# Kernel optimization log

Hardware: AMD Instinct MI355X
Metric: run time of the kernel (lower is better)

## Reference

```python
import jax, jax.numpy as jnp
import numpy as np

B, S, E, H = 2, 2048, 1024, 16
HD = E // H
SCALE = 1.0 / np.sqrt(HD)
PR_QKV = 0.05   # precision_ratio for q/k/v (critical_attention=False)
PR_OUT = 0.10
ROUTE_THR = 0.05  # gradient_threshold (critical_attention=False)
LN_EPS = 1e-5


def rpb_linear(x, W, b, precision_ratio):
    """ResidualPrecisionBoostLinear: ternary-quantized weight (threshold 0.7*mean|W|,
    per-tensor scale) plus top-`precision_ratio` fraction of residual kept full precision."""
    absW = jnp.abs(W)
    thr = 0.7 * jnp.mean(absW)
    tmask = (absW > thr).astype(W.dtype)
    scale = jnp.sum(absW * tmask) / jnp.maximum(jnp.sum(tmask), 1.0)
    Wq = scale * jnp.sign(W) * tmask
    res = W - Wq
    k = int(precision_ratio * W.size)
    kth = jax.lax.top_k(jnp.abs(res).ravel(), k)[0][-1]
    W_eff = Wq + res * (jnp.abs(res) >= kth).astype(W.dtype)
    return x @ W_eff.T + b


def selective_route(x, threshold):
    # forward: zero out small-magnitude activations (straight-through in training)
    return x * (jnp.abs(x) >= threshold).astype(x.dtype)


def layer_norm(x, g, b):
    mu = jnp.mean(x, axis=-1, keepdims=True)
    var = jnp.mean(jnp.square(x - mu), axis=-1, keepdims=True)
    return (x - mu) * jax.lax.rsqrt(var + LN_EPS) * g + b


def setup_inputs() -> dict:
    key = jax.random.key(0)
    ks = jax.random.split(key, 12)
    f = lambda k, shp, s=1.0: jax.random.normal(k, shp, dtype=jnp.float32) * s
    return {
        "query": f(ks[0], (B, S, E)),
        "key": f(ks[1], (B, S, E)),
        "value": f(ks[2], (B, S, E)),
        "Wq": f(ks[3], (E, E), 0.02), "bq": jnp.zeros((E,), jnp.float32),
        "Wk": f(ks[4], (E, E), 0.02), "bk": jnp.zeros((E,), jnp.float32),
        "Wv": f(ks[5], (E, E), 0.02), "bv": jnp.zeros((E,), jnp.float32),
        "Wo": f(ks[6], (E, E), 0.02), "bo": jnp.zeros((E,), jnp.float32),
        "ln_g": jnp.ones((E,), jnp.float32),
        "ln_b": jnp.zeros((E,), jnp.float32),
    }


def reference(query, key, value, Wq, bq, Wk, bk, Wv, bv, Wo, bo, ln_g, ln_b):
    qn = layer_norm(query, ln_g, ln_b)
    q = selective_route(rpb_linear(qn, Wq, bq, PR_QKV), ROUTE_THR)
    k = selective_route(rpb_linear(key, Wk, bk, PR_QKV), ROUTE_THR)
    v = selective_route(rpb_linear(value, Wv, bv, PR_QKV), ROUTE_THR)
    # [B,S,E] -> [B,H,S,HD]
    q = q.reshape(B, S, H, HD).transpose(0, 2, 1, 3)
    k = k.reshape(B, S, H, HD).transpose(0, 2, 1, 3)
    v = v.reshape(B, S, H, HD).transpose(0, 2, 1, 3)
    scores = jnp.einsum("bhqd,bhkd->bhqk", q, k) * SCALE
    attn = jax.nn.softmax(scores, axis=-1)   # dropout is identity in eval
    ctx = jnp.einsum("bhqk,bhkd->bhqd", attn, v)
    ctx = ctx.transpose(0, 2, 1, 3).reshape(B, S, E)
    return rpb_linear(ctx, Wo, bo, PR_OUT)
```

## Files before the change

kernel.cpp:

```cpp
#include <hip/hip_runtime.h>
#include <stdio.h>
#include <stdint.h>

#define BB 2
#define SS 2048
#define ED 1024
#define HH 16
#define HDD 64
#define MROWS 4096
#define NW_ELEM 1048576u

typedef unsigned short ushortT;
typedef __attribute__((ext_vector_type(8))) short bf16x8;
typedef __attribute__((ext_vector_type(4))) float f32x4;
typedef __attribute__((ext_vector_type(16))) float f32x16;

#define U_WHI 0u
#define U_WLO 4194304u
#define U_XQ  8388608u
#define U_XK  12582912u
#define U_XV  16777216u
#define U_QH  20971520u
#define U_KH  25165824u
#define U_VH  29360128u
#define LP_OFF  33554432u
#define P0_OFF  67108864u
#define P1_OFF  83886080u
#define SMALL_OFF  100663296u
#define HIST_OFF   SMALL_OFF
#define ABS_OFF    (SMALL_OFF + 16384u)
#define MSK_OFF    (ABS_OFF + 32u)
#define CNT_OFF    (MSK_OFF + 32u)
#define SMALL_BYTES 16464u
#define WS_NEEDED  (SMALL_OFF + SMALL_BYTES)

#define SC44 17592186044416.0f
#define INV44 (1.0 / 17592186044416.0)
#define QSCALE 0.18033688011112042f

__device__ __forceinline__ const float* wsel(int w, const float* W0, const float* W1,
                                             const float* W2, const float* W3) {
  return w == 0 ? W0 : w == 1 ? W1 : w == 2 ? W2 : W3;
}

__device__ __forceinline__ ushortT f2bf(float x) {
  unsigned u = __float_as_uint(x);
  unsigned r = (u + 0x7FFFu + ((u >> 16) & 1u)) >> 16;
  return (ushortT)r;
}
__device__ __forceinline__ float bf2f(ushortT b) {
  return __uint_as_float(((unsigned)b) << 16);
}
__device__ __forceinline__ void bsplit(float x, ushortT& h, ushortT& l) {
  ushortT hb = f2bf(x);
  float hf = bf2f(hb);
  h = hb;
  l = f2bf(x - hf);
}
__device__ __forceinline__ unsigned pkbf(float a, float b) {
  unsigned r;
  asm("v_cvt_pk_bf16_f32 %0, %1, %2" : "=v"(r) : "v"(a), "v"(b));
  return r;
}
__device__ __forceinline__ void plswap(unsigned& a, unsigned& b) {
  asm("v_permlane32_swap_b32 %0, %1" : "+v"(a), "+v"(b));
}
__device__ __forceinline__ float fexp2(float x) {
#if __has_builtin(__builtin_amdgcn_exp2f)
  return __builtin_amdgcn_exp2f(x);
#else
  float r;
  asm("v_exp_f32 %0, %1\n\ts_nop 1" : "=v"(r) : "v"(x));
  return r;
#endif
}

__device__ __forceinline__ void gld_lds16(const ushortT* g, ushortT* s) {
  __builtin_amdgcn_global_load_lds((__attribute__((address_space(1))) void*)g,
                                   (__attribute__((address_space(3))) void*)s, 16, 0, 0);
}

template <int N> __device__ __forceinline__ void waitv() {
  if constexpr (N == 0) asm volatile("s_waitcnt vmcnt(0)" ::: "memory");
  else if constexpr (N == 4) asm volatile("s_waitcnt vmcnt(4)" ::: "memory");
  else if constexpr (N == 6) asm volatile("s_waitcnt vmcnt(6)" ::: "memory");
}
__device__ __forceinline__ void pipe_barrier() {
  __builtin_amdgcn_s_barrier();
  __builtin_amdgcn_sched_barrier(0);
}

__device__ __forceinline__ float get_thr(const unsigned long long* sAbs, int w) {
  return 0.7f * (float)((double)sAbs[w] * INV44 / 1048576.0);
}
__device__ __forceinline__ float get_scale(const unsigned long long* sMsk,
                                           const unsigned* cnt, int w) {
  double s = (double)sMsk[w] * INV44;
  return (float)s / fmaxf((float)cnt[w], 1.0f);
}

__device__ __forceinline__ void scan_sel(const unsigned* hist, unsigned& k, unsigned& prefix,
                                         unsigned* sh, int t) {
  sh[t] = hist[t];
  __syncthreads();
  for (int off = 1; off < 256; off <<= 1) {
    unsigned add = (t + off < 256) ? sh[t + off] : 0u;
    __syncthreads();
    sh[t] += add;
    __syncthreads();
  }
  int sel = __syncthreads_count((int)(sh[t] >= k)) - 1;
  unsigned suf = sh[sel];
  k -= (suf - hist[sel]);
  prefix = (prefix << 8) | (unsigned)sel;
  __syncthreads();
}

__device__ __forceinline__ void ln_unit(const float* __restrict__ query,
                                        const float* __restrict__ g,
                                        const float* __restrict__ b,
                                        ushortT* __restrict__ Xq,
                                        int row, int t, float* red) {
  float4 v = *(const float4*)&query[(size_t)row * ED + t * 4];
  float s = v.x + v.y + v.z + v.w;
#pragma unroll
  for (int m = 32; m; m >>= 1) s += __shfl_xor(s, m, 64);
  if ((t & 63) == 0) red[t >> 6] = s;
  __syncthreads();
  float mu = (red[0] + red[1] + red[2] + red[3]) * (1.0f / 1024.0f);
  float dx = v.x - mu, dy = v.y - mu, dz = v.z - mu, dw = v.w - mu;
  float s2 = dx * dx + dy * dy + dz * dz + dw * dw;
#pragma unroll
  for (int m = 32; m; m >>= 1) s2 += __shfl_xor(s2, m, 64);
  if ((t & 63) == 0) red[4 + (t >> 6)] = s2;
  __syncthreads();
  float var = (red[4] + red[5] + red[6] + red[7]) * (1.0f / 1024.0f);
  float inv = rsqrtf(var + 1e-5f);
  float4 gg = *(const float4*)&g[t * 4];
  float4 bb = *(const float4*)&b[t * 4];
  float ys[4] = {dx * inv * gg.x + bb.x, dy * inv * gg.y + bb.y,
                 dz * inv * gg.z + bb.z, dw * inv * gg.w + bb.w};
  ushort4 h4;
#pragma unroll
  for (int c = 0; c < 4; c++) ((ushortT*)&h4)[c] = f2bf(ys[c]);
  *(ushort4*)&Xq[(size_t)row * ED + t * 4] = h4;
}

__device__ __forceinline__ void cast_unit(const float* __restrict__ src,
                                          ushortT* __restrict__ dst, int idx, int t) {
  const int i = (idx * 256 + t) * 4;
  float4 v = *(const float4*)&src[i];
  ushort4 h4;
  h4.x = f2bf(v.x); h4.y = f2bf(v.y); h4.z = f2bf(v.z); h4.w = f2bf(v.w);
  *(ushort4*)&dst[i] = h4;
}

__global__ __launch_bounds__(256) void k_pre(const float* __restrict__ query,
                                             const float* __restrict__ key,
                                             const float* __restrict__ value,
                                             const float* __restrict__ g,
                                             const float* __restrict__ b,
                                             const float* W0, const float* W1,
                                             const float* W2, const float* W3,
                                             ushortT* __restrict__ Xq,
                                             ushortT* __restrict__ Xk,
                                             ushortT* __restrict__ Xv,
                                             unsigned long long* sAbs) {
  const int t = threadIdx.x, bid = blockIdx.x;
  __shared__ float red[8];
  __shared__ unsigned long long sd[256];
  if (bid < 4096) {
    ln_unit(query, g, b, Xq, bid, t, red);
  } else if (bid < 8192) {
    cast_unit(key, Xk, bid - 4096, t);
  } else if (bid < 12288) {
    cast_unit(value, Xv, bid - 8192, t);
  } else {
    const int c = bid - 12288, w = c >> 8;
    const float* W = wsel(w, W0, W1, W2, W3) + (c & 255) * 4096;
    unsigned long long s = 0;
#pragma unroll
    for (int r = 0; r < 4; r++) {
      float4 v = *(const float4*)(W + (t + 256 * r) * 4);
      s += (unsigned long long)(fabsf(v.x) * SC44);
      s += (unsigned long long)(fabsf(v.y) * SC44);
      s += (unsigned long long)(fabsf(v.z) * SC44);
      s += (unsigned long long)(fabsf(v.w) * SC44);
    }
    sd[t] = s;
    __syncthreads();
    for (int off = 128; off > 0; off >>= 1) {
      if (t < off) sd[t] += sd[t + off];
      __syncthreads();
    }
    if (!t) atomicAdd(&sAbs[w], sd[0]);
  }
}

__global__ __launch_bounds__(256) void k_masked(const float* W0, const float* W1,
                                                const float* W2, const float* W3,
                                                const unsigned long long* sAbs,
                                                unsigned long long* sMsk, unsigned* sCnt) {
  const int w = blockIdx.y, t = threadIdx.x;
  const float thr = get_thr(sAbs, w);
  const float* W = wsel(w, W0, W1, W2, W3) + blockIdx.x * 4096;
  unsigned long long s = 0;
  unsigned c = 0;
#pragma unroll
  for (int r = 0; r < 4; r++) {
    float4 v = *(const float4*)(W + (t + 256 * r) * 4);
    float xs[4] = {v.x, v.y, v.z, v.w};
#pragma unroll
    for (int q = 0; q < 4; q++) {
      float a = fabsf(xs[q]);
      if (a > thr) { s += (unsigned long long)(a * SC44); c++; }
    }
  }
  __shared__ unsigned long long sd[256];
  __shared__ unsigned sc[256];
  sd[t] = s; sc[t] = c;
  __syncthreads();
  for (int off = 128; off > 0; off >>= 1) {
    if (t < off) { sd[t] += sd[t + off]; sc[t] += sc[t + off]; }
    __syncthreads();
  }
  if (!t) { atomicAdd(&sMsk[w], sd[0]); atomicAdd(&sCnt[w], sc[0]); }
}

__global__ __launch_bounds__(256) void k_hist(const float* W0, const float* W1,
                                              const float* W2, const float* W3,
                                              const unsigned long long* sAbs,
                                              const unsigned long long* sMsk,
                                              const unsigned* sCnt,
                                              unsigned* histG, int pass) {
  const int w = blockIdx.y, t = threadIdx.x;
  __shared__ unsigned sh[256];
  __shared__ unsigned h[256];
  const float thr = get_thr(sAbs, w);
  const float scale = get_scale(sMsk, sCnt, w);
  unsigned k = (w == 3) ? 104857u : 52428u, prefix = 0u;
  for (int pp = 0; pp < pass; pp++)
    scan_sel(histG + (pp * 4 + w) * 256, k, prefix, sh, t);

  h[t] = 0;
  __syncthreads();
  const float* W = wsel(w, W0, W1, W2, W3) + blockIdx.x * 4096;
  const int shift1 = 32 - 8 * pass;
  const int shift2 = 24 - 8 * pass;
#pragma unroll
  for (int r = 0; r < 4; r++) {
    float4 v = *(const float4*)(W + (t + 256 * r) * 4);
    float xs[4] = {v.x, v.y, v.z, v.w};
#pragma unroll
    for (int q = 0; q < 4; q++) {
      float x = xs[q];
      float a = fabsf(x);
      float wq = (a > thr) ? copysignf(scale, x) : 0.0f;
      unsigned bits = __float_as_uint(fabsf(x - wq));
      if (pass == 0) {
        atomicAdd(&h[bits >> 24], 1u);
      } else {
        if ((bits >> shift1) == prefix)
          atomicAdd(&h[(bits >> shift2) & 255u], 1u);
      }
    }
  }
  __syncthreads();
  if (h[t]) atomicAdd(&histG[(pass * 4 + w) * 256 + t], h[t]);
}

__global__ __launch_bounds__(256) void k_weff(const float* W0, const float* W1,
                                              const float* W2, const float* W3,
                                              const unsigned long long* sAbs,
                                              const unsigned long long* sMsk,
                                              const unsigned* sCnt,
                                              const unsigned* histG,
                                              ushortT* Whi, ushortT* Wlo) {
  const int w = blockIdx.y, t = threadIdx.x;
  __shared__ unsigned sh[256];
  const float thr = get_thr(sAbs, w);
  const float scale = get_scale(sMsk, sCnt, w);
  unsigned k = (w == 3) ? 104857u : 52428u, kth = 0u;
  for (int pp = 0; pp < 4; pp++)
    scan_sel(histG + (pp * 4 + w) * 256, k, kth, sh, t);

  const unsigned idx = (blockIdx.x * 256 + t) * 4;
  const float* W = wsel(w, W0, W1, W2, W3);
  float4 v = *(const float4*)(W + idx);
  float xs[4] = {v.x, v.y, v.z, v.w};
  ushort4 h4, l4;
#pragma unroll
  for (int c = 0; c < 4; c++) {
    float x = xs[c];
    float a = fabsf(x);
    float wq = (a > thr) ? copysignf(scale, x) : 0.0f;
    float res = x - wq;
    unsigned bits = __float_as_uint(fabsf(res));
    float we = wq + ((bits >= kth) ? res : 0.0f);
    ushortT hh, ll;
    bsplit(we, hh, ll);
    ((ushortT*)&h4)[c] = hh;
    ((ushortT*)&l4)[c] = ll;
  }
  *(ushort4*)&Whi[(size_t)w * NW_ELEM + idx] = h4;
  *(ushort4*)&Wlo[(size_t)w * NW_ELEM + idx] = l4;
}

__device__ __forceinline__ f32x4 mfma16(bf16x8 a, bf16x8 b, f32x4 c) {
  return __builtin_amdgcn_mfma_f32_16x16x32_bf16(a, b, c, 0, 0, 0);
}

template <int MODE, bool ALO, bool WLO, int BK, int MINW>
__global__ __launch_bounds__(256, MINW) void k_gemmP(
    const ushortT* __restrict__ A0, const ushortT* __restrict__ A0l,
    const ushortT* __restrict__ A1,
    const ushortT* __restrict__ Wh, const ushortT* __restrict__ Wl,
    const float* __restrict__ bias0, const float* __restrict__ bias1,
    ushortT* __restrict__ Cb0, ushortT* __restrict__ Cb1,
    float* __restrict__ Cf) {
  constexpr int ABUF = (BK == 64) ? 8192 : 4096;
  constexpr int BBUF = (BK == 64) ? 4096 : 2048;
  constexpr int L = ((BK == 64) ? 4 : 2) * (1 + (ALO ? 1 : 0)) +
                    ((BK == 64) ? 2 : 1) * (1 + (WLO ? 1 : 0));
  constexpr int NT = 1024 / BK;
  __shared__ __align__(16) ushortT sAh[3 * ABUF];
  __shared__ __align__(16) ushortT sAl[ALO ? 3 * ABUF : 8];
  __shared__ __align__(16) ushortT sBh[3 * BBUF];
  __shared__ __align__(16) ushortT sBl[WLO ? 3 * BBUF : 8];

  const int t = threadIdx.x;
  const int w = t >> 6, l = t & 63;
  const int wr = w >> 1, wc = w & 1;

  const int which = (MODE == 0) ? (blockIdx.x >> 9) : 0;
  const int wid = blockIdx.x & 511;
  int id2 = (wid & 7) * 64 + (wid >> 3);
  const int m0 = (id2 >> 4) * 128, n0 = (id2 & 15) * 64;

  const ushortT* A = (MODE == 0 && which) ? A1 : A0;
  const ushortT* Wha = Wh + (MODE == 0 ? (unsigned)which * NW_ELEM : 0u);
  const float* bias = (MODE == 0 && which) ? bias1 : bias0;

  const int sr = l >> 3, swz = (l & 7) ^ sr;
  const int srow = l >> 2, sgr = (l & 3) ^ ((l >> 3) & 3);

  auto stage = [&](int kt, int buf) {
    if constexpr (BK == 64) {
#pragma unroll
      for (int s2 = 0; s2 < 4; s2++) {
        int seg = w * 4 + s2;
        size_t ga = (size_t)(m0 + seg * 8 + sr) * ED + kt * 64 + swz * 8;
        gld_lds16(A + ga, sAh + buf * ABUF + seg * 512);
        if constexpr (ALO) gld_lds16(A0l + ga, sAl + buf * ABUF + seg * 512);
      }
#pragma unroll
      for (int s2 = 0; s2 < 2; s2++) {
        int seg = w * 2 + s2;
        size_t gb = (size_t)(n0 + seg * 8 + sr) * ED + kt * 64 + swz * 8;
        gld_lds16(Wha + gb, sBh + buf * BBUF + seg * 512);
        if constexpr (WLO) gld_lds16(Wl + gb, sBl + buf * BBUF + seg * 512);
      }
    } else {
#pragma unroll
      for (int s2 = 0; s2 < 2; s2++) {
        int seg = w * 2 + s2;
        size_t ga = (size_t)(m0 + seg * 16 + srow) * ED + kt * 32 + sgr * 8;
        gld_lds16(A + ga, sAh + buf * ABUF + seg * 512);
        if constexpr (ALO) gld_lds16(A0l + ga, sAl + buf * ABUF + seg * 512);
      }
      {
        size_t gb = (size_t)(n0 + w * 16 + srow) * ED + kt * 32 + sgr * 8;
        gld_lds16(Wha + gb, sBh + buf * BBUF + w * 512);
        if constexpr (WLO) gld_lds16(Wl + gb, sBl + buf * BBUF + w * 512);
      }
    }
  };

  f32x4 acc[4][2];
#pragma unroll
  for (int i = 0; i < 4; i++)
#pragma unroll
    for (int j = 0; j < 2; j++) acc[i][j] = (f32x4){0.0f, 0.0f, 0.0f, 0.0f};

  auto compute = [&](int buf) {
    if constexpr (BK == 64) {
#pragma unroll
      for (int ks = 0; ks < 2; ks++) {
        bf16x8 ah[4], al[4], bh2[2], bl2[2];
        const int G = ks * 4 + (l >> 4);
#pragma unroll
        for (int i = 0; i < 4; i++) {
          int r = wr * 64 + i * 16 + (l & 15);
          int off = buf * ABUF + r * 64 + ((G ^ (l & 7)) << 3);
          ah[i] = *(const bf16x8*)&sAh[off];
          if constexpr (ALO) al[i] = *(const bf16x8*)&sAl[off];
        }
#pragma unroll
        for (int j = 0; j < 2; j++) {
          int r = wc * 32 + j * 16 + (l & 15);
          int off = buf * BBUF + r * 64 + ((G ^ (l & 7)) << 3);
          bh2[j] = *(const bf16x8*)&sBh[off];
          if constexpr (WLO) bl2[j] = *(const bf16x8*)&sBl[off];
        }
#pragma unroll
        for (int i = 0; i < 4; i++)
#pragma unroll
          for (int j = 0; j < 2; j++) {
            acc[i][j] = mfma16(ah[i], bh2[j], acc[i][j]);
            if constexpr (WLO) acc[i][j] = mfma16(ah[i], bl2[j], acc[i][j]);
            if constexpr (ALO) acc[i][j] = mfma16(al[i], bh2[j], acc[i][j]);
          }
      }
    } else {
      bf16x8 ah[4], al[4], bh2[2], bl2[2];
      const int G = l >> 4;
#pragma unroll
      for (int i = 0; i < 4; i++) {
        int r = wr * 64 + i * 16 + (l & 15);
        int off = buf * ABUF + r * 32 + ((G ^ ((r >> 1) & 3)) << 3);
        ah[i] = *(const bf16x8*)&sAh[off];
        if constexpr (ALO) al[i] = *(const bf16x8*)&sAl[off];
      }
#pragma unroll
      for (int j = 0; j < 2; j++) {
        int r = wc * 32 + j * 16 + (l & 15);
        int off = buf * BBUF + r * 32 + ((G ^ ((r >> 1) & 3)) << 3);
        bh2[j] = *(const bf16x8*)&sBh[off];
        if constexpr (WLO) bl2[j] = *(const bf16x8*)&sBl[off];
      }
#pragma unroll
      for (int i = 0; i < 4; i++)
#pragma unroll
        for (int j = 0; j < 2; j++) {
          acc[i][j] = mfma16(ah[i], bh2[j], acc[i][j]);
          if constexpr (WLO) acc[i][j] = mfma16(ah[i], bl2[j], acc[i][j]);
          if constexpr (ALO) acc[i][j] = mfma16(al[i], bh2[j], acc[i][j]);
        }
    }
  };

  stage(0, 0);
  stage(1, 1);
  for (int kt = 0; kt < NT; ++kt) {
    if (kt < NT - 1) waitv<L>(); else waitv<0>();
    pipe_barrier();
    if (kt + 2 < NT) stage(kt + 2, (kt + 2) % 3);
    __builtin_amdgcn_s_setprio(1);
    compute(kt % 3);
    __builtin_amdgcn_s_setprio(0);
  }

  const int coln = l & 15, row4 = (l >> 4) * 4;
  float bn[2];
#pragma unroll
  for (int j = 0; j < 2; j++) bn[j] = bias[n0 + wc * 32 + j * 16 + coln];
  const int b_ = m0 >> 11, h_ = n0 >> 6;

  if constexpr (MODE == 1) {
#pragma unroll
    for (int i = 0; i < 4; i++)
#pragma unroll
      for (int j = 0; j < 2; j++) {
        int n = n0 + wc * 32 + j * 16 + coln;
#pragma unroll
        for (int r = 0; r < 4; r++) {
          int m = m0 + wr * 64 + i * 16 + row4 + r;
          Cf[(size_t)m * ED + n] = acc[i][j][r] + bn[j];
        }
      }
  } else if constexpr (MODE == 0) {
    const float osc = (which == 0) ? QSCALE : 1.0f;
    ushortT* C = which ? Cb1 : Cb0;
#pragma unroll
    for (int i = 0; i < 4; i++)
#pragma unroll
      for (int j = 0; j < 2; j++) {
        int hd = wc * 32 + j * 16 + coln;
#pragma unroll
        for (int r = 0; r < 4; r++) {
          int m = m0 + wr * 64 + i * 16 + row4 + r;
          int s_ = m & 2047;
          float y = acc[i][j][r] + bn[j];
          y = (fabsf(y) >= 0.05f) ? y : 0.0f;
          y *= osc;
          C[((size_t)(b_ * HH + h_) * SS + s_) * HDD + hd] = f2bf(y);
        }
      }
  } else {
#pragma unroll
    for (int i = 0; i < 4; i++)
#pragma unroll
      for (int j = 0; j < 2; j++) {
        int hd = wc * 32 + j * 16 + coln;
        int s0_ = (m0 + wr * 64 + i * 16 + row4) & 2047;
        ushort4 h4;
#pragma unroll
        for (int r = 0; r < 4; r++) {
          float y = acc[i][j][r] + bn[j];
          y = (fabsf(y) >= 0.05f) ? y : 0.0f;
          ((ushortT*)&h4)[r] = f2bf(y);
        }
        *(ushort4*)&Cb0[((size_t)(b_ * HH + h_) * HDD + hd) * SS + s0_] = h4;
      }
  }
}

__device__ __forceinline__ f32x16 mfma32(bf16x8 a, bf16x8 b, f32x16 c) {
  return __builtin_amdgcn_mfma_f32_32x32x16_bf16(a, b, c, 0, 0, 0);
}

__device__ __forceinline__ void exppack(const f32x16& A, float* ls4,
                                        bf16x8& paA, bf16x8& paB) {
  float p[16];
#pragma unroll
  for (int r = 0; r < 16; r++) {
    p[r] = fexp2(A[r]);
    ls4[r & 3] += p[r];
  }
  unsigned c0 = pkbf(p[0], p[1]), c1 = pkbf(p[2], p[3]);
  unsigned c2 = pkbf(p[4], p[5]), c3 = pkbf(p[6], p[7]);
  unsigned c4 = pkbf(p[8], p[9]), c5 = pkbf(p[10], p[11]);
  unsigned c6 = pkbf(p[12], p[13]), c7 = pkbf(p[14], p[15]);
  plswap(c0, c2); plswap(c1, c3); plswap(c4, c6); plswap(c5, c7);
  uint4 ta = make_uint4(c0, c1, c2, c3);
  uint4 tb = make_uint4(c4, c5, c6, c7);
  paA = __builtin_bit_cast(bf16x8, ta);
  paB = __builtin_bit_cast(bf16x8, tb);
}

__global__ __launch_bounds__(256, 4) void k_attn(
    const ushortT* __restrict__ Qh, const ushortT* __restrict__ Kh,
    const ushortT* __restrict__ Vh,
    float* __restrict__ Pp, float* __restrict__ Lp) {
  __shared__ __align__(16) ushortT sK[2 * 4096];
  __shared__ __align__(16) ushortT sV[2 * 4096];

  const int t = threadIdx.x;
  const int w = t >> 6, l = t & 63;
  const int l32 = l & 31, g = l >> 5;

  int id = blockIdx.x;
  int id2 = (id & 7) * 128 + (id >> 3);
  const int bh = id2 >> 5;
  const int qt = (id2 >> 1) & 15;
  const int half = id2 & 1;

  const size_t kqbase = (size_t)bh * (SS * HDD);
  const size_t vbase = (size_t)bh * (HDD * SS);
  const int q0 = qt * 128 + w * 32;
  const int sbase = half * 1024;

  bf16x8 qh[4];
  const size_t qrow = kqbase + (size_t)(q0 + l32) * HDD;
#pragma unroll
  for (int ks = 0; ks < 4; ks++) qh[ks] = *(const bf16x8*)&Qh[qrow + ks * 16 + g * 8];

  f32x16 octx0, octx1;
#pragma unroll
  for (int i = 0; i < 16; i++) { octx0[i] = 0.0f; octx1[i] = 0.0f; }
  float ls4[4] = {0.0f, 0.0f, 0.0f, 0.0f};

  const int srow = l >> 3;
  const int sgr = (l & 7) ^ srow;

  auto stageA = [&](int kt, int buf) {
    const int s0 = sbase + kt * 64;
#pragma unroll
    for (int s2 = 0; s2 < 2; s2++) {
      int seg = w * 2 + s2;
      int row = seg * 8 + srow;
      gld_lds16(Kh + kqbase + (size_t)(s0 + row) * HDD + sgr * 8, sK + buf * 4096 + seg * 512);
      gld_lds16(Vh + vbase + (size_t)row * SS + s0 + sgr * 8, sV + buf * 4096 + seg * 512);
    }
  };

  stageA(0, 0);
  __syncthreads();

  for (int kt = 0; kt < 16; ++kt) {
    if (kt < 15) stageA(kt + 1, (kt + 1) & 1);
    const ushortT* cK = sK + (kt & 1) * 4096;
    const ushortT* cV = sV + (kt & 1) * 4096;

    f32x16 acc0, acc1;
#pragma unroll
    for (int i = 0; i < 16; i++) { acc0[i] = 0.0f; acc1[i] = 0.0f; }
#pragma unroll
    for (int ks = 0; ks < 4; ks++) {
      int sw = ((ks * 2 + g) ^ (l32 & 7)) << 3;
      bf16x8 kh0 = *(const bf16x8*)&cK[l32 * 64 + sw];
      bf16x8 kh1 = *(const bf16x8*)&cK[(32 + l32) * 64 + sw];
      acc0 = mfma32(kh0, qh[ks], acc0);
      acc1 = mfma32(kh1, qh[ks], acc1);
    }

    bf16x8 pa0, pa1, pa2, pa3;
    exppack(acc0, ls4, pa0, pa1);
    exppack(acc1, ls4, pa2, pa3);

#pragma unroll
    for (int js = 0; js < 4; js++) {
      bf16x8 pj = js == 0 ? pa0 : js == 1 ? pa1 : js == 2 ? pa2 : pa3;
      int vsw = ((js * 2 + g) ^ (l32 & 7)) << 3;
      bf16x8 vh0 = *(const bf16x8*)&cV[l32 * 64 + vsw];
      bf16x8 vh1 = *(const bf16x8*)&cV[(32 + l32) * 64 + vsw];
      octx0 = mfma32(pj, vh0, octx0);
      octx1 = mfma32(pj, vh1, octx1);
    }
    __syncthreads();
  }

  float lsum = (ls4[0] + ls4[1]) + (ls4[2] + ls4[3]);
  float ls = lsum + __shfl_xor(lsum, 32, 64);
  if (g == 0) Lp[half * 65536 + bh * 2048 + q0 + l32] = ls;

  float* P = Pp + (size_t)half * 4194304u;
#pragma unroll
  for (int r = 0; r < 16; r++) {
    int q = (r & 3) + 8 * (r >> 2) + 4 * g;
    size_t pb = ((size_t)bh * 2048 + q0 + q) * 64;
    P[pb + l32] = octx0[r];
    P[pb + 32 + l32] = octx1[r];
  }
}

__global__ __launch_bounds__(256) void k_reduce(const float* __restrict__ Pp,
                                                const float* __restrict__ Lp,
                                                ushortT* __restrict__ ctxH,
                                                ushortT* __restrict__ ctxL) {
  const unsigned i4 = (blockIdx.x * 256 + threadIdx.x) * 4;
  const int d = i4 & 63;
  const int sq = (i4 >> 6) & 2047;
  const int bh = i4 >> 17;
  float ls = Lp[bh * 2048 + sq] + Lp[65536 + bh * 2048 + sq];
  float inv = 1.0f / ls;
  float4 a = *(const float4*)&Pp[i4];
  float4 b = *(const float4*)&Pp[4194304u + i4];
  float os[4] = {(a.x + b.x) * inv, (a.y + b.y) * inv,
                 (a.z + b.z) * inv, (a.w + b.w) * inv};
  ushort4 h4, l4;
#pragma unroll
  for (int c = 0; c < 4; c++) {
    ushortT hh, ll;
    bsplit(os[c], hh, ll);
    ((ushortT*)&h4)[c] = hh;
    ((ushortT*)&l4)[c] = ll;
  }
  size_t ci = ((size_t)((bh >> 4) * 2048 + sq)) * 1024 + (bh & 15) * 64 + d;
  *(ushort4*)&ctxH[ci] = h4;
  *(ushort4*)&ctxL[ci] = l4;
}

extern "C" void kernel_launch(void* const* d_in, const int* in_sizes, int n_in,
                              void* d_out, int out_size, void* d_ws, size_t ws_size,
                              hipStream_t stream) {
  const float* query = (const float*)d_in[0];
  const float* key   = (const float*)d_in[1];
  const float* value = (const float*)d_in[2];
  const float* Wq = (const float*)d_in[3];
  const float* bq = (const float*)d_in[4];
  const float* Wk = (const float*)d_in[5];
  const float* bk = (const float*)d_in[6];
  const float* Wv = (const float*)d_in[7];
  const float* bv = (const float*)d_in[8];
  const float* Wo = (const float*)d_in[9];
  const float* bo = (const float*)d_in[10];
  const float* lng = (const float*)d_in[11];
  const float* lnb = (const float*)d_in[12];
  float* out = (float*)d_out;

  if (ws_size < (size_t)WS_NEEDED) {
    fprintf(stderr, "kernel_launch: ws too small (%zu < %u)\n", ws_size, WS_NEEDED);
    return;
  }

  ushortT* wsu = (ushortT*)d_ws;
  ushortT* Whi = wsu + U_WHI;
  ushortT* Wlo = wsu + U_WLO;
  ushortT* Xq  = wsu + U_XQ;
  ushortT* Xk  = wsu + U_XK;
  ushortT* Xv  = wsu + U_XV;
  ushortT* Qhp = wsu + U_QH;
  ushortT* Khp = wsu + U_KH;
  ushortT* Vhp = wsu + U_VH;
  ushortT* Chp = wsu + U_XQ;
  ushortT* Clp = wsu + U_XK;

  char* wsb = (char*)d_ws;
  float* Pp = (float*)(wsb + P0_OFF);
  float* Lp = (float*)(wsb + LP_OFF);
  unsigned* histG = (unsigned*)(wsb + HIST_OFF);
  unsigned long long* sAbs = (unsigned long long*)(wsb + ABS_OFF);
  unsigned long long* sMsk = (unsigned long long*)(wsb + MSK_OFF);
  unsigned* sCnt = (unsigned*)(wsb + CNT_OFF);

  hipMemsetAsync(histG, 0, SMALL_BYTES, stream);

  k_pre<<<13312, 256, 0, stream>>>(query, key, value, lng, lnb,
                                   Wq, Wk, Wv, Wo, Xq, Xk, Xv, sAbs);

  dim3 gW(256, 4);
  k_masked<<<gW, 256, 0, stream>>>(Wq, Wk, Wv, Wo, sAbs, sMsk, sCnt);
  for (int pass = 0; pass < 4; ++pass)
    k_hist<<<gW, 256, 0, stream>>>(Wq, Wk, Wv, Wo, sAbs, sMsk, sCnt, histG, pass);
  k_weff<<<dim3(1024, 4), 256, 0, stream>>>(Wq, Wk, Wv, Wo, sAbs, sMsk, sCnt, histG,
                                            Whi, Wlo);

  k_gemmP<0, false, false, 64, 2><<<1024, 256, 0, stream>>>(
      Xq, nullptr, Xk, Whi, nullptr, bq, bk, Qhp, Khp, nullptr);
  k_gemmP<2, false, true, 32, 3><<<512, 256, 0, stream>>>(
      Xv, nullptr, nullptr, Whi + 2 * NW_ELEM, Wlo + 2 * NW_ELEM, bv, nullptr,
      Vhp, nullptr, nullptr);

  k_attn<<<1024, 256, 0, stream>>>(Qhp, Khp, Vhp, Pp, Lp);
  k_reduce<<<4096, 256, 0, stream>>>(Pp, Lp, Chp, Clp);

  k_gemmP<1, true, true, 32, 2><<<512, 256, 0, stream>>>(
      Chp, Clp, nullptr, Whi + 3 * NW_ELEM, Wlo + 3 * NW_ELEM, bo, nullptr,
      nullptr, nullptr, out);
}
```

Baseline: 240.9 us.

## Use 12/12/8-bit radix passes for top-k threshold selection

Replaces the four 8-bit radix-select histogram passes with three passes of 12, 12 and 8 bits. Each pass now uses 4096-bin shared histograms and a two-level scan, and the weight kernels launch twice as many blocks, each handling half the elements. This removes one full read of the weight matrices and one kernel launch, but makes each scan heavier and adds global atomics per block when flushing the larger histograms. The histogram buffer moves into the P0 workspace region, which the attention kernel overwrites later.

Result: slower. 258.3 us (+7.2%).

```diff
diff --git a/kernel.cpp b/kernel.cpp
--- a/kernel.cpp
+++ b/kernel.cpp
@@ -26,13 +26,12 @@
 #define LP_OFF  33554432u
 #define P0_OFF  67108864u
 #define P1_OFF  83886080u
+#define HIST_BYTES 135168u
 #define SMALL_OFF  100663296u
-#define HIST_OFF   SMALL_OFF
-#define ABS_OFF    (SMALL_OFF + 16384u)
-#define MSK_OFF    (ABS_OFF + 32u)
-#define CNT_OFF    (MSK_OFF + 32u)
-#define SMALL_BYTES 16464u
-#define WS_NEEDED  (SMALL_OFF + SMALL_BYTES)
+#define ABS_OFF    SMALL_OFF
+#define MSK_OFF    (SMALL_OFF + 32u)
+#define CNT_OFF    (SMALL_OFF + 64u)
+#define WS_NEEDED  (SMALL_OFF + 96u)
 
 #define SC44 17592186044416.0f
 #define INV44 (1.0 / 17592186044416.0)
@@ -99,9 +98,14 @@
   return (float)s / fmaxf((float)cnt[w], 1.0f);
 }
 
-__device__ __forceinline__ void scan_sel(const unsigned* hist, unsigned& k, unsigned& prefix,
-                                         unsigned* sh, int t) {
-  sh[t] = hist[t];
+__device__ __forceinline__ unsigned scan_sel4k(const unsigned* hist, unsigned& k,
+                                               unsigned* sh, int t) {
+  unsigned loc[16];
+  unsigned tsum = 0;
+#pragma unroll
+  for (int i = 0; i < 16; i++) { loc[i] = hist[t * 16 + i]; tsum += loc[i]; }
+  __syncthreads();
+  sh[t] = tsum;
   __syncthreads();
   for (int off = 1; off < 256; off <<= 1) {
     unsigned add = (t + off < 256) ? sh[t + off] : 0u;
@@ -109,11 +113,43 @@
     sh[t] += add;
     __syncthreads();
   }
+  int selt = __syncthreads_count((int)(sh[t] >= k)) - 1;
+  if (t == selt) {
+    unsigned cum = (selt < 255) ? sh[selt + 1] : 0u;
+    unsigned kk = k;
+    int bi = 0;
+#pragma unroll 1
+    for (int i = 15; i >= 0; --i) {
+      cum += loc[i];
+      if (cum >= kk) { bi = i; kk = kk - (cum - loc[i]); break; }
+    }
+    sh[0] = (unsigned)(selt * 16 + bi);
+    sh[1] = kk;
+  }
+  __syncthreads();
+  unsigned sel = sh[0];
+  k = sh[1];
+  __syncthreads();
+  return sel;
+}
+
+__device__ __forceinline__ unsigned scan_sel256(const unsigned* hist, unsigned& k,
+                                                unsigned* sh, int t) {
+  unsigned myv = hist[t];
+  __syncthreads();
+  sh[t] = myv;
+  __syncthreads();
+  for (int off = 1; off < 256; off <<= 1) {
+    unsigned add = (t + off < 256) ? sh[t + off] : 0u;
+    __syncthreads();
+    sh[t] += add;
+    __syncthreads();
+  }
   int sel = __syncthreads_count((int)(sh[t] >= k)) - 1;
   unsigned suf = sh[sel];
   k -= (suf - hist[sel]);
-  prefix = (prefix << 8) | (unsigned)sel;
-  __syncthreads();
+  __syncthreads();
+  return (unsigned)sel;
 }
 
 __device__ __forceinline__ void ln_unit(const float* __restrict__ query,
@@ -203,11 +239,11 @@
                                                 unsigned long long* sMsk, unsigned* sCnt) {
   const int w = blockIdx.y, t = threadIdx.x;
   const float thr = get_thr(sAbs, w);
-  const float* W = wsel(w, W0, W1, W2, W3) + blockIdx.x * 4096;
+  const float* W = wsel(w, W0, W1, W2, W3) + blockIdx.x * 2048;
   unsigned long long s = 0;
   unsigned c = 0;
 #pragma unroll
-  for (int r = 0; r < 4; r++) {
+  for (int r = 0; r < 2; r++) {
     float4 v = *(const float4*)(W + (t + 256 * r) * 4);
     float xs[4] = {v.x, v.y, v.z, v.w};
 #pragma unroll
@@ -227,28 +263,34 @@
   if (!t) { atomicAdd(&sMsk[w], sd[0]); atomicAdd(&sCnt[w], sc[0]); }
 }
 
-__global__ __launch_bounds__(256) void k_hist(const float* W0, const float* W1,
-                                              const float* W2, const float* W3,
-                                              const unsigned long long* sAbs,
-                                              const unsigned long long* sMsk,
-                                              const unsigned* sCnt,
-                                              unsigned* histG, int pass) {
+template <int PASS>
+__global__ __launch_bounds__(256) void k_histP(const float* W0, const float* W1,
+                                               const float* W2, const float* W3,
+                                               const unsigned long long* sAbs,
+                                               const unsigned long long* sMsk,
+                                               const unsigned* sCnt,
+                                               unsigned* histG) {
+  constexpr int NB = (PASS == 2) ? 256 : 4096;
   const int w = blockIdx.y, t = threadIdx.x;
   __shared__ unsigned sh[256];
-  __shared__ unsigned h[256];
+  __shared__ unsigned hl[NB];
   const float thr = get_thr(sAbs, w);
   const float scale = get_scale(sMsk, sCnt, w);
-  unsigned k = (w == 3) ? 104857u : 52428u, prefix = 0u;
-  for (int pp = 0; pp < pass; pp++)
-    scan_sel(histG + (pp * 4 + w) * 256, k, prefix, sh, t);
-
-  h[t] = 0;
-  __syncthreads();
-  const float* W = wsel(w, W0, W1, W2, W3) + blockIdx.x * 4096;
-  const int shift1 = 32 - 8 * pass;
-  const int shift2 = 24 - 8 * pass;
-#pragma unroll
-  for (int r = 0; r < 4; r++) {
+  unsigned* H0 = histG + w * 4096;
+  unsigned* H1 = histG + 4 * 4096 + w * 4096;
+  unsigned* H2 = histG + 8 * 4096 + w * 256;
+
+  unsigned k = (w == 3) ? 104857u : 52428u;
+  unsigned prefix = 0;
+  if constexpr (PASS >= 1) prefix = scan_sel4k(H0, k, sh, t);
+  if constexpr (PASS >= 2) prefix = (prefix << 12) | scan_sel4k(H1, k, sh, t);
+
+  for (int i = t; i < NB; i += 256) hl[i] = 0;
+  __syncthreads();
+
+  const float* W = wsel(w, W0, W1, W2, W3) + blockIdx.x * 2048;
+#pragma unroll
+  for (int r = 0; r < 2; r++) {
     float4 v = *(const float4*)(W + (t + 256 * r) * 4);
     float xs[4] = {v.x, v.y, v.z, v.w};
 #pragma unroll
@@ -257,16 +299,19 @@
       float a = fabsf(x);
       float wq = (a > thr) ? copysignf(scale, x) : 0.0f;
       unsigned bits = __float_as_uint(fabsf(x - wq));
-      if (pass == 0) {
-        atomicAdd(&h[bits >> 24], 1u);
+      if constexpr (PASS == 0) {
+        atomicAdd(&hl[bits >> 20], 1u);
+      } else if constexpr (PASS == 1) {
+        if ((bits >> 20) == prefix) atomicAdd(&hl[(bits >> 8) & 4095u], 1u);
       } else {
-        if ((bits >> shift1) == prefix)
-          atomicAdd(&h[(bits >> shift2) & 255u], 1u);
-      }
-    }
-  }
-  __syncthreads();
-  if (h[t]) atomicAdd(&histG[(pass * 4 + w) * 256 + t], h[t]);
+        if ((bits >> 8) == prefix) atomicAdd(&hl[bits & 255u], 1u);
+      }
+    }
+  }
+  __syncthreads();
+  unsigned* HG = (PASS == 0) ? H0 : (PASS == 1) ? H1 : H2;
+  for (int i = t; i < NB; i += 256)
+    if (hl[i]) atomicAdd(&HG[i], hl[i]);
 }
 
 __global__ __launch_bounds__(256) void k_weff(const float* W0, const float* W1,
@@ -280,9 +325,14 @@
   __shared__ unsigned sh[256];
   const float thr = get_thr(sAbs, w);
   const float scale = get_scale(sMsk, sCnt, w);
-  unsigned k = (w == 3) ? 104857u : 52428u, kth = 0u;
-  for (int pp = 0; pp < 4; pp++)
-    scan_sel(histG + (pp * 4 + w) * 256, k, kth, sh, t);
+  const unsigned* H0 = histG + w * 4096;
+  const unsigned* H1 = histG + 4 * 4096 + w * 4096;
+  const unsigned* H2 = histG + 8 * 4096 + w * 256;
+  unsigned k = (w == 3) ? 104857u : 52428u;
+  unsigned p0 = scan_sel4k(H0, k, sh, t);
+  unsigned p1 = scan_sel4k(H1, k, sh, t);
+  unsigned p2 = scan_sel256(H2, k, sh, t);
+  const unsigned kth = (((p0 << 12) | p1) << 8) | p2;
 
   const unsigned idx = (blockIdx.x * 256 + t) * 4;
   const float* W = wsel(w, W0, W1, W2, W3);
@@ -689,20 +739,21 @@
   char* wsb = (char*)d_ws;
   float* Pp = (float*)(wsb + P0_OFF);
   float* Lp = (float*)(wsb + LP_OFF);
-  unsigned* histG = (unsigned*)(wsb + HIST_OFF);
+  unsigned* histG = (unsigned*)(wsb + P0_OFF);
   unsigned long long* sAbs = (unsigned long long*)(wsb + ABS_OFF);
   unsigned long long* sMsk = (unsigned long long*)(wsb + MSK_OFF);
   unsigned* sCnt = (unsigned*)(wsb + CNT_OFF);
 
-  hipMemsetAsync(histG, 0, SMALL_BYTES, stream);
+  hipMemsetAsync(histG, 0, HIST_BYTES, stream);
+  hipMemsetAsync(wsb + ABS_OFF, 0, 96, stream);
 
   k_pre<<<13312, 256, 0, stream>>>(query, key, value, lng, lnb,
                                    Wq, Wk, Wv, Wo, Xq, Xk, Xv, sAbs);
 
-  dim3 gW(256, 4);
-  k_masked<<<gW, 256, 0, stream>>>(Wq, Wk, Wv, Wo, sAbs, sMsk, sCnt);
-  for (int pass = 0; pass < 4; ++pass)
-    k_hist<<<gW, 256, 0, stream>>>(Wq, Wk, Wv, Wo, sAbs, sMsk, sCnt, histG, pass);
+  k_masked<<<dim3(512, 4), 256, 0, stream>>>(Wq, Wk, Wv, Wo, sAbs, sMsk, sCnt);
+  k_histP<0><<<dim3(512, 4), 256, 0, stream>>>(Wq, Wk, Wv, Wo, sAbs, sMsk, sCnt, histG);
+  k_histP<1><<<dim3(512, 4), 256, 0, stream>>>(Wq, Wk, Wv, Wo, sAbs, sMsk, sCnt, histG);
+  k_histP<2><<<dim3(512, 4), 256, 0, stream>>>(Wq, Wk, Wv, Wo, sAbs, sMsk, sCnt, histG);
   k_weff<<<dim3(1024, 4), 256, 0, stream>>>(Wq, Wk, Wv, Wo, sAbs, sMsk, sCnt, histG,
                                             Whi, Wlo);
 
```

## Compact radix-select candidates after second pass to shrink later histogram passes

Applied to the files above, without the earlier changes.

The radix top-k threshold search previously rescanned all four weight matrices in each of four histogram passes. Now pass 1 also writes the residual bits that match the top-byte prefix into a compact buffer, and passes 2 and 3 build their histograms only from that buffer. This cuts global weight reads and recomputation of the quantized residual in the last two passes. In exchange it adds a shared-memory staging buffer of 16KB per block plus global atomics for the compaction, and the pass 1 kernel may run with lower occupancy.

Measured after the change: 252.1 us. 1.05x slower.

```diff
diff --git a/kernel.cpp b/kernel.cpp
--- a/kernel.cpp
+++ b/kernel.cpp
@@ -31,7 +31,8 @@
 #define ABS_OFF    (SMALL_OFF + 16384u)
 #define MSK_OFF    (ABS_OFF + 32u)
 #define CNT_OFF    (MSK_OFF + 32u)
-#define SMALL_BYTES 16464u
+#define CCNT_OFF   (CNT_OFF + 16u)
+#define SMALL_BYTES 16480u
 #define WS_NEEDED  (SMALL_OFF + SMALL_BYTES)
 
 #define SC44 17592186044416.0f
@@ -227,26 +228,19 @@
   if (!t) { atomicAdd(&sMsk[w], sd[0]); atomicAdd(&sCnt[w], sc[0]); }
 }
 
-__global__ __launch_bounds__(256) void k_hist(const float* W0, const float* W1,
-                                              const float* W2, const float* W3,
-                                              const unsigned long long* sAbs,
-                                              const unsigned long long* sMsk,
-                                              const unsigned* sCnt,
-                                              unsigned* histG, int pass) {
+__global__ __launch_bounds__(256) void k_hist0(const float* W0, const float* W1,
+                                               const float* W2, const float* W3,
+                                               const unsigned long long* sAbs,
+                                               const unsigned long long* sMsk,
+                                               const unsigned* sCnt,
+                                               unsigned* histG) {
   const int w = blockIdx.y, t = threadIdx.x;
-  __shared__ unsigned sh[256];
   __shared__ unsigned h[256];
   const float thr = get_thr(sAbs, w);
   const float scale = get_scale(sMsk, sCnt, w);
-  unsigned k = (w == 3) ? 104857u : 52428u, prefix = 0u;
-  for (int pp = 0; pp < pass; pp++)
-    scan_sel(histG + (pp * 4 + w) * 256, k, prefix, sh, t);
-
   h[t] = 0;
   __syncthreads();
   const float* W = wsel(w, W0, W1, W2, W3) + blockIdx.x * 4096;
-  const int shift1 = 32 - 8 * pass;
-  const int shift2 = 24 - 8 * pass;
 #pragma unroll
   for (int r = 0; r < 4; r++) {
     float4 v = *(const float4*)(W + (t + 256 * r) * 4);
@@ -257,16 +251,90 @@
       float a = fabsf(x);
       float wq = (a > thr) ? copysignf(scale, x) : 0.0f;
       unsigned bits = __float_as_uint(fabsf(x - wq));
-      if (pass == 0) {
-        atomicAdd(&h[bits >> 24], 1u);
-      } else {
-        if ((bits >> shift1) == prefix)
-          atomicAdd(&h[(bits >> shift2) & 255u], 1u);
-      }
-    }
-  }
-  __syncthreads();
-  if (h[t]) atomicAdd(&histG[(pass * 4 + w) * 256 + t], h[t]);
+      atomicAdd(&h[bits >> 24], 1u);
+    }
+  }
+  __syncthreads();
+  if (h[t]) atomicAdd(&histG[w * 256 + t], h[t]);
+}
+
+__global__ __launch_bounds__(256) void k_hist1(const float* W0, const float* W1,
+                                               const float* W2, const float* W3,
+                                               const unsigned long long* sAbs,
+                                               const unsigned long long* sMsk,
+                                               const unsigned* sCnt,
+                                               unsigned* histG,
+                                               unsigned* cbuf, unsigned* ccnt) {
+  const int w = blockIdx.y, t = threadIdx.x;
+  __shared__ unsigned sh[256];
+  __shared__ unsigned h[256];
+  __shared__ unsigned sbuf[4096];
+  __shared__ unsigned cloc, cbase;
+  const float thr = get_thr(sAbs, w);
+  const float scale = get_scale(sMsk, sCnt, w);
+  unsigned k = (w == 3) ? 104857u : 52428u, prefix = 0u;
+  scan_sel(histG + w * 256, k, prefix, sh, t);
+
+  h[t] = 0;
+  if (!t) cloc = 0;
+  __syncthreads();
+  const float* W = wsel(w, W0, W1, W2, W3) + blockIdx.x * 4096;
+#pragma unroll
+  for (int r = 0; r < 4; r++) {
+    float4 v = *(const float4*)(W + (t + 256 * r) * 4);
+    float xs[4] = {v.x, v.y, v.z, v.w};
+#pragma unroll
+    for (int q = 0; q < 4; q++) {
+      float x = xs[q];
+      float a = fabsf(x);
+      float wq = (a > thr) ? copysignf(scale, x) : 0.0f;
+      unsigned bits = __float_as_uint(fabsf(x - wq));
+      if ((bits >> 24) == prefix) {
+        atomicAdd(&h[(bits >> 16) & 255u], 1u);
+        unsigned p = atomicAdd(&cloc, 1u);
+        sbuf[p] = bits;
+      }
+    }
+  }
+  __syncthreads();
+  if (h[t]) atomicAdd(&histG[(4 + w) * 256 + t], h[t]);
+  if (!t) cbase = atomicAdd(&ccnt[w], cloc);
+  __syncthreads();
+  const unsigned n = cloc, base = w * NW_ELEM + cbase;
+  for (unsigned i = t; i < n; i += 256) cbuf[base + i] = sbuf[i];
+}
+
+template <int PASS>
+__global__ __launch_bounds__(256) void k_histC(const unsigned* histG_ro,
+                                               unsigned* histG,
+                                               const unsigned* cbuf,
+                                               const unsigned* ccnt) {
+  const int w = blockIdx.y, t = threadIdx.x;
+  __shared__ unsigned sh[256];
+  __shared__ unsigned h[256];
+  unsigned k = (w == 3) ? 104857u : 52428u, prefix = 0u;
+  scan_sel(histG_ro + w * 256, k, prefix, sh, t);
+  scan_sel(histG_ro + (4 + w) * 256, k, prefix, sh, t);
+  unsigned p1 = prefix & 255u, p2 = 0;
+  if constexpr (PASS == 3) {
+    scan_sel(histG_ro + (8 + w) * 256, k, prefix, sh, t);
+    p2 = prefix & 255u;
+  }
+  h[t] = 0;
+  __syncthreads();
+  const unsigned n = ccnt[w];
+  const unsigned* cb = cbuf + w * NW_ELEM;
+  for (unsigned i = blockIdx.x * 256 + t; i < n; i += 64 * 256) {
+    unsigned bits = cb[i];
+    if constexpr (PASS == 2) {
+      if (((bits >> 16) & 255u) == p1) atomicAdd(&h[(bits >> 8) & 255u], 1u);
+    } else {
+      if (((bits >> 16) & 255u) == p1 && ((bits >> 8) & 255u) == p2)
+        atomicAdd(&h[bits & 255u], 1u);
+    }
+  }
+  __syncthreads();
+  if (h[t]) atomicAdd(&histG[(PASS * 4 + w) * 256 + t], h[t]);
 }
 
 __global__ __launch_bounds__(256) void k_weff(const float* W0, const float* W1,
@@ -689,10 +757,12 @@
   char* wsb = (char*)d_ws;
   float* Pp = (float*)(wsb + P0_OFF);
   float* Lp = (float*)(wsb + LP_OFF);
+  unsigned* cbuf = (unsigned*)(wsb + P1_OFF);
   unsigned* histG = (unsigned*)(wsb + HIST_OFF);
   unsigned long long* sAbs = (unsigned long long*)(wsb + ABS_OFF);
   unsigned long long* sMsk = (unsigned long long*)(wsb + MSK_OFF);
   unsigned* sCnt = (unsigned*)(wsb + CNT_OFF);
+  unsigned* ccnt = (unsigned*)(wsb + CCNT_OFF);
 
   hipMemsetAsync(histG, 0, SMALL_BYTES, stream);
 
@@ -701,8 +771,10 @@
 
   dim3 gW(256, 4);
   k_masked<<<gW, 256, 0, stream>>>(Wq, Wk, Wv, Wo, sAbs, sMsk, sCnt);
-  for (int pass = 0; pass < 4; ++pass)
-    k_hist<<<gW, 256, 0, stream>>>(Wq, Wk, Wv, Wo, sAbs, sMsk, sCnt, histG, pass);
+  k_hist0<<<gW, 256, 0, stream>>>(Wq, Wk, Wv, Wo, sAbs, sMsk, sCnt, histG);
+  k_hist1<<<gW, 256, 0, stream>>>(Wq, Wk, Wv, Wo, sAbs, sMsk, sCnt, histG, cbuf, ccnt);
+  k_histC<2><<<dim3(64, 4), 256, 0, stream>>>(histG, histG, cbuf, ccnt);
+  k_histC<3><<<dim3(64, 4), 256, 0, stream>>>(histG, histG, cbuf, ccnt);
   k_weff<<<dim3(1024, 4), 256, 0, stream>>>(Wq, Wk, Wv, Wo, sAbs, sMsk, sCnt, histG,
                                             Whi, Wlo);
 
```
